# Optimization experiments

Measured on AMD Instinct MI355X. Metric: run time of the kernel, lower is better.

## Reference

```python
import jax, jax.numpy as jnp
from jax import lax
import numpy as np

DN = ('NCHW', 'OIHW', 'NCHW')


def conv3x3(x, w, b):
    y = lax.conv_general_dilated(x, w, (1, 1), ((1, 1), (1, 1)), dimension_numbers=DN)
    return y + b[None, :, None, None]


def box_mean(x, k):
    # Uniform k x k box mean with reflect padding; separable (exactly equal to
    # the dense ones/k^2 conv in the original since the kernel is rank-1).
    pad = k // 2
    C = x.shape[1]
    xp = jnp.pad(x, ((0, 0), (0, 0), (pad, pad), (pad, pad)), mode='reflect')
    kh = jnp.ones((C, 1, k, 1), x.dtype) / k
    kw = jnp.ones((C, 1, 1, k), x.dtype) / k
    y = lax.conv_general_dilated(xp, kh, (1, 1), 'VALID', feature_group_count=C, dimension_numbers=DN)
    y = lax.conv_general_dilated(y, kw, (1, 1), 'VALID', feature_group_count=C, dimension_numbers=DN)
    return y


def std_map_for_window(features, k):
    # features: [N, 8, H, W]
    C = features.shape[1]
    m = box_mean(features, k)
    m2 = box_mean(features * features, k)
    var = jnp.maximum(m2 - m * m, 1e-6)
    w = jax.nn.softmax(jnp.ones((C,), features.dtype))  # uniform (C==8 branch)
    sm = jnp.einsum('nchw,c->nhw', jnp.sqrt(var), w)[:, None]  # [N,1,H,W]
    return jnp.power(sm, 0.8)


def setup_inputs() -> dict:
    key = jax.random.key(0)
    ks = jax.random.split(key, 8)
    B, H, W = 8, 512, 512
    x = jax.random.normal(ks[0], (B, 4, H, W), dtype=jnp.float32)
    s = 0.05
    conv1_w = jax.random.normal(ks[1], (32, 4, 3, 3), jnp.float32) * s
    conv1_b = jnp.zeros((32,), jnp.float32)
    conv2_w = jax.random.normal(ks[2], (16, 32, 3, 3), jnp.float32) * s
    conv2_b = jnp.zeros((16,), jnp.float32)
    conv3_w = jax.random.normal(ks[3], (8, 16, 3, 3), jnp.float32) * s
    conv3_b = jnp.zeros((8,), jnp.float32)
    fusion_w = jnp.full((1, 3, 1, 1), 1.0 / 3.0, jnp.float32)  # init per module
    fusion_b = jnp.zeros((1,), jnp.float32)
    channel_weights = jnp.ones((4,), jnp.float32) / 4.0
    return dict(x=x, conv1_w=conv1_w, conv1_b=conv1_b, conv2_w=conv2_w,
                conv2_b=conv2_b, conv3_w=conv3_w, conv3_b=conv3_b,
                fusion_w=fusion_w, fusion_b=fusion_b,
                channel_weights=channel_weights)


def reference(x, conv1_w, conv1_b, conv2_w, conv2_b, conv3_w, conv3_b,
              fusion_w, fusion_b, channel_weights):
    window_sizes = (11, 25, 49)
    # feature extractor
    f = jax.nn.leaky_relu(conv3x3(x, conv1_w, conv1_b), 0.2)
    f = jax.nn.leaky_relu(conv3x3(f, conv2_w, conv2_b), 0.2)
    f = conv3x3(f, conv3_w, conv3_b)  # [B,8,H,W]
    # multi-scale std maps
    maps = [std_map_for_window(f, k) for k in window_sizes]
    multi = jnp.concatenate(maps, axis=1)  # [B,3,H,W]
    fused = jax.nn.relu(
        lax.conv_general_dilated(multi, fusion_w, (1, 1), 'VALID', dimension_numbers=DN)
        + fusion_b[None, :, None, None])  # [B,1,H,W]
    # adaptive thresholds
    std_flat = fused.ravel()
    q = jnp.quantile(std_flat, jnp.array([0.25, 0.75], fused.dtype))
    q25, q75 = q[0], q[1]
    iqr = q75 - q25
    iqr = jnp.where(iqr < 1e-5, jnp.asarray(0.05, fused.dtype), iqr)
    global_std = jnp.std(x, axis=(2, 3), keepdims=True, ddof=1)  # [B,4,1,1]
    lower = jnp.broadcast_to((q25 - 0.5 * iqr), global_std.shape)
    upper = jnp.broadcast_to((q75 + 0.5 * iqr), global_std.shape)
    gf = jnp.clip(global_std * 5.0, 0.5, 2.0)
    lower = lower * gf
    upper = upper * gf
    cw = jax.nn.softmax(channel_weights).reshape(1, 4, 1, 1)
    channel_std = jnp.std(x * cw, axis=(2, 3), keepdims=True, ddof=1)
    cf = jnp.clip(channel_std * 2.0, 0.8, 1.2)
    lower = lower * cf
    upper = upper * cf
    degenerate = jnp.min(jnp.abs(upper - lower)) < 1e-5
    mean_t = (upper + lower) / 2
    lower = jnp.where(degenerate, mean_t - 0.05, lower)
    upper = jnp.where(degenerate, mean_t + 0.05, upper)
    # texture mask
    diff = jnp.maximum(upper - lower, 1e-5)
    norm = jnp.clip((fused - lower) / diff, 0.0, 1.0)  # [B,4,H,W] via broadcast
    mask = jax.nn.sigmoid(6.0 * norm - 3.0)
    return jnp.mean(mask, axis=1, keepdims=True)  # [B,1,H,W]
```

## Files before the change

### kernel.cpp

```cpp
#include <hip/hip_runtime.h>
#include <hip/hip_bf16.h>
#include <math.h>


template<int CIN, int COUT, int COT, bool LRELU>
__global__ __launch_bounds__(256) void conv3x3_k(
    const float* __restrict__ in,
    const float* __restrict__ wgt,
    const float* __restrict__ bias,
    float* __restrict__ out)
{
    constexpr int TW = 64, TH = 32, CG = COUT / COT, SW = TW + 4;
    __shared__ float sl[(TH + 2) * SW];

    const int tx  = threadIdx.x & 7;
    const int ty  = threadIdx.x >> 3;
    const int x0  = blockIdx.x * TW;
    const int y0  = blockIdx.y * TH;
    const int cog = blockIdx.z % CG;
    const int bb  = blockIdx.z / CG;

    const float* inb = in + (size_t)bb * CIN * 512 * 512;

    float acc[COT][8];
#pragma unroll
    for (int j = 0; j < COT; ++j)
#pragma unroll
        for (int p = 0; p < 8; ++p) acc[j][p] = 0.f;

    for (int ci = 0; ci < CIN; ++ci) {
        __syncthreads();
        const float* ip = inb + (size_t)ci * 512 * 512;
        for (int idx = threadIdx.x; idx < (TH + 2) * (TW + 2); idx += 256) {
            int r  = idx / (TW + 2);
            int cc = idx - r * (TW + 2);
            int yy = y0 - 1 + r, xx = x0 - 1 + cc;
            float v = 0.f;
            if ((unsigned)yy < 512u && (unsigned)xx < 512u) v = ip[yy * 512 + xx];
            sl[r * SW + cc] = v;
        }
        __syncthreads();
        const float* wci = wgt + ((size_t)(cog * COT) * CIN + ci) * 9;
#pragma unroll
        for (int dy = 0; dy < 3; ++dy) {
            const float* rowp = &sl[(ty + dy) * SW + tx * 8];
            float rr[10];
            float4 a0 = *(const float4*)(rowp);
            float4 a1 = *(const float4*)(rowp + 4);
            float2 a2 = *(const float2*)(rowp + 8);
            rr[0]=a0.x; rr[1]=a0.y; rr[2]=a0.z; rr[3]=a0.w;
            rr[4]=a1.x; rr[5]=a1.y; rr[6]=a1.z; rr[7]=a1.w;
            rr[8]=a2.x; rr[9]=a2.y;
#pragma unroll
            for (int j = 0; j < COT; ++j) {
#pragma unroll
                for (int dx = 0; dx < 3; ++dx) {
                    float w = wci[(size_t)j * CIN * 9 + dy * 3 + dx];
#pragma unroll
                    for (int p = 0; p < 8; ++p)
                        acc[j][p] = fmaf(rr[p + dx], w, acc[j][p]);
                }
            }
        }
    }

    const int y = y0 + ty;
#pragma unroll
    for (int j = 0; j < COT; ++j) {
        int co = cog * COT + j;
        float b = bias[co];
        float* op = out + (((size_t)bb * COUT + co) * 512 + y) * 512 + x0 + tx * 8;
        float v[8];
#pragma unroll
        for (int p = 0; p < 8; ++p) {
            float t = acc[j][p] + b;
            if (LRELU) t = t > 0.f ? t : 0.2f * t;
            v[p] = t;
        }
        ((float4*)op)[0] = make_float4(v[0], v[1], v[2], v[3]);
        ((float4*)op)[1] = make_float4(v[4], v[5], v[6], v[7]);
    }
}

__device__ __forceinline__ float2 f2add(float2 a, float2 b) {
    return make_float2(a.x + b.x, a.y + b.y);
}
__device__ __forceinline__ int mir(int v) {
    return v < 0 ? -v : (v > 511 ? 1022 - v : v);
}

#define YB 4

__global__ __launch_bounds__(256) void stdmap_k(
    const float* __restrict__ f,
    const float* __restrict__ fw,
    const float* __restrict__ fbp,
    float* __restrict__ fused,
    int b0)
{
    const int y0   = blockIdx.x * YB;
    const int bb   = blockIdx.y;
    const int t    = threadIdx.x;
    const int lane = t & 63, wid = t >> 6;

    __shared__ float S[3][2][513];
    __shared__ float wtt[4][6];

    const int   RAD[3] = {5, 12, 24};
    const float INV[3] = {1.f/121.f, 1.f/625.f, 1.f/2401.f};

    float smacc[3][YB][2];
#pragma unroll
    for (int sc = 0; sc < 3; ++sc)
#pragma unroll
        for (int yy = 0; yy < YB; ++yy)
            { smacc[sc][yy][0] = 0.f; smacc[sc][yy][1] = 0.f; }

    for (int c = 0; c < 8; ++c) {
        const float* base = f + ((size_t)bb * 8 + c) * 512 * 512;

        float2 wf[3], wq[3];
        {
            float2 sf[3] = {{0.f,0.f},{0.f,0.f},{0.f,0.f}};
            float2 sq[3] = {{0.f,0.f},{0.f,0.f},{0.f,0.f}};
#pragma unroll
            for (int dy = -24; dy <= 24; ++dy) {
                int row = mir(y0 + dy);
                float2 v  = ((const float2*)(base + (size_t)row * 512))[t];
                float2 vq = make_float2(v.x * v.x, v.y * v.y);
                int ad = dy < 0 ? -dy : dy;
                int ring = ad <= 5 ? 0 : (ad <= 12 ? 1 : 2);
                sf[ring] = f2add(sf[ring], v);
                sq[ring] = f2add(sq[ring], vq);
            }
            wf[0] = sf[0];              wq[0] = sq[0];
            wf[1] = f2add(sf[1], wf[0]); wq[1] = f2add(sq[1], wq[0]);
            wf[2] = f2add(sf[2], wf[1]); wq[2] = f2add(sq[2], wq[1]);
        }

        for (int yy = 0; yy < YB; ++yy) {
            const int y = y0 + yy;
            if (yy > 0) {
#pragma unroll
                for (int sc = 0; sc < 3; ++sc) {
                    int ra = mir(y + RAD[sc]);
                    int rs = mir(y - 1 - RAD[sc]);
                    float2 va = ((const float2*)(base + (size_t)ra * 512))[t];
                    float2 vs = ((const float2*)(base + (size_t)rs * 512))[t];
                    wf[sc].x += va.x - vs.x;       wf[sc].y += va.y - vs.y;
                    wq[sc].x += va.x*va.x - vs.x*vs.x;
                    wq[sc].y += va.y*va.y - vs.y*vs.y;
                }
            }

            float pf[3], pq[3], incf[3], incq[3];
#pragma unroll
            for (int sc = 0; sc < 3; ++sc) {
                pf[sc] = wf[sc].x + wf[sc].y;
                pq[sc] = wq[sc].x + wq[sc].y;
                incf[sc] = pf[sc]; incq[sc] = pq[sc];
            }
#pragma unroll
            for (int off = 1; off < 64; off <<= 1) {
#pragma unroll
                for (int sc = 0; sc < 3; ++sc) {
                    float uf = __shfl_up(incf[sc], (unsigned)off, 64);
                    float uq = __shfl_up(incq[sc], (unsigned)off, 64);
                    if (lane >= off) { incf[sc] += uf; incq[sc] += uq; }
                }
            }
            if (lane == 63) {
#pragma unroll
                for (int sc = 0; sc < 3; ++sc) {
                    wtt[wid][sc]     = incf[sc];
                    wtt[wid][3 + sc] = incq[sc];
                }
            }
            __syncthreads();
            float wpf[3] = {0.f,0.f,0.f}, wpq[3] = {0.f,0.f,0.f};
#pragma unroll
            for (int w = 0; w < 4; ++w)
                if (w < wid)
#pragma unroll
                    for (int sc = 0; sc < 3; ++sc) {
                        wpf[sc] += wtt[w][sc];
                        wpq[sc] += wtt[w][3 + sc];
                    }
#pragma unroll
            for (int sc = 0; sc < 3; ++sc) {
                float exf = wpf[sc] + incf[sc] - pf[sc];
                float exq = wpq[sc] + incq[sc] - pq[sc];
                S[sc][0][2*t+1] = exf + wf[sc].x;
                S[sc][0][2*t+2] = exf + pf[sc];
                S[sc][1][2*t+1] = exq + wq[sc].x;
                S[sc][1][2*t+2] = exq + pq[sc];
            }
            if (t == 0)
#pragma unroll
                for (int sc = 0; sc < 3; ++sc)
                    { S[sc][0][0] = 0.f; S[sc][1][0] = 0.f; }
            __syncthreads();

#pragma unroll
            for (int sc = 0; sc < 3; ++sc) {
                const int r = RAD[sc];
                const float* Sf = S[sc][0];
                const float* Sq = S[sc][1];
#pragma unroll
                for (int slot = 0; slot < 2; ++slot) {
                    int xx = 2*t + slot;
                    int lo = xx - r, hi = xx + r;
                    int loc = lo < 0 ? 0 : lo;
                    int hic = hi > 511 ? 511 : hi;
                    float wfv = Sf[hic + 1] - Sf[loc];
                    float wqv = Sq[hic + 1] - Sq[loc];
                    if (lo < 0)   { wfv += Sf[r - xx + 1] - Sf[1];
                                    wqv += Sq[r - xx + 1] - Sq[1]; }
                    if (hi > 511) { wfv += Sf[511] - Sf[1022 - xx - r];
                                    wqv += Sq[511] - Sq[1022 - xx - r]; }
                    float m   = wfv * INV[sc];
                    float m2  = wqv * INV[sc];
                    float var = m2 - m * m;
                    var = var > 1e-6f ? var : 1e-6f;
                    smacc[sc][yy][slot] += sqrtf(var);
                }
            }
            __syncthreads();
        }
    }

    const float w0 = fw[0], w1 = fw[1], w2 = fw[2], b = fbp[0];
#pragma unroll
    for (int yy = 0; yy < YB; ++yy) {
        float o[2];
#pragma unroll
        for (int slot = 0; slot < 2; ++slot) {
            float m0 = powf(smacc[0][yy][slot] * 0.125f, 0.8f);
            float m1 = powf(smacc[1][yy][slot] * 0.125f, 0.8f);
            float m2 = powf(smacc[2][yy][slot] * 0.125f, 0.8f);
            float fv = w0 * m0 + w1 * m1 + w2 * m2 + b;
            o[slot] = fv > 0.f ? fv : 0.f;
        }
        ((float2*)(fused + ((size_t)(b0 + bb) * 512 + y0 + yy) * 512))[t] =
            make_float2(o[0], o[1]);
    }
}

__global__ __launch_bounds__(256) void plane_std_part_k(
    const float* __restrict__ x, double* __restrict__ part)
{
    const int plane = blockIdx.x >> 5;
    const int blk   = blockIdx.x & 31;
    const float* p = x + (size_t)plane * 262144 + (size_t)blk * 8192;
    double s = 0.0, s2 = 0.0;
    for (int i = threadIdx.x; i < 2048; i += 256) {
        float4 v = ((const float4*)p)[i];
        s  += (double)v.x + (double)v.y + (double)v.z + (double)v.w;
        s2 += (double)v.x * v.x + (double)v.y * v.y
            + (double)v.z * v.z + (double)v.w * v.w;
    }
    __shared__ double ls[256], ls2[256];
    ls[threadIdx.x] = s; ls2[threadIdx.x] = s2;
    __syncthreads();
    for (int off = 128; off > 0; off >>= 1) {
        if (threadIdx.x < off) {
            ls[threadIdx.x]  += ls[threadIdx.x + off];
            ls2[threadIdx.x] += ls2[threadIdx.x + off];
        }
        __syncthreads();
    }
    if (threadIdx.x == 0) {
        part[2 * blockIdx.x]     = ls[0];
        part[2 * blockIdx.x + 1] = ls2[0];
    }
}

__global__ void plane_std_fin_k(const double* __restrict__ part,
                                float* __restrict__ stds)
{
    const int plane = threadIdx.x;
    if (plane >= 32) return;
    double s = 0.0, s2 = 0.0;
    for (int b = 0; b < 32; ++b) {
        s  += part[2 * (plane * 32 + b)];
        s2 += part[2 * (plane * 32 + b) + 1];
    }
    const double N = 262144.0;
    double var = (s2 - s * s / N) / (N - 1.0);
    stds[plane] = (float)sqrt(var > 0.0 ? var : 0.0);
}

__global__ __launch_bounds__(256) void hist1_k(
    const float* __restrict__ fused, unsigned* __restrict__ h)
{
    __shared__ unsigned lh[4096];
    for (int i = threadIdx.x; i < 4096; i += 256) lh[i] = 0u;
    __syncthreads();
    const int base = blockIdx.x * 2048;
    for (int i = threadIdx.x; i < 2048; i += 256) {
        unsigned bits = __float_as_uint(fused[base + i]);
        atomicAdd(&lh[bits >> 20], 1u);
    }
    __syncthreads();
    for (int i = threadIdx.x; i < 4096; i += 256) {
        unsigned c = lh[i];
        if (c) atomicAdd(&h[i], c);
    }
}

__global__ __launch_bounds__(256) void select_par_k(
    const unsigned* __restrict__ h, unsigned* __restrict__ pfx,
    unsigned* __restrict__ rem, int level)
{
    const int tt = blockIdx.x;
    const int t = threadIdx.x, lane = t & 63, wid = t >> 6;
    const unsigned targets[4] = {524287u, 524288u, 1572863u, 1572864u};
    const unsigned R = (level == 1) ? targets[tt] : rem[tt];
    const unsigned* hb = (level == 1) ? h : h + tt * 4096;

    unsigned loc[16], lsum = 0;
    const uint4* hv = (const uint4*)(hb + t * 16);
#pragma unroll
    for (int i = 0; i < 4; ++i) {
        uint4 v = hv[i];
        loc[4*i]=v.x; loc[4*i+1]=v.y; loc[4*i+2]=v.z; loc[4*i+3]=v.w;
        lsum += v.x + v.y + v.z + v.w;
    }
    __shared__ unsigned warr[4];
    __shared__ unsigned rbin, rrem;
    unsigned inc = lsum;
#pragma unroll
    for (int off = 1; off < 64; off <<= 1) {
        unsigned up = __shfl_up(inc, (unsigned)off, 64);
        if (lane >= off) inc += up;
    }
    if (lane == 63) warr[wid] = inc;
    __syncthreads();
    unsigned wpre = 0;
#pragma unroll
    for (int w = 0; w < 4; ++w) if (w < wid) wpre += warr[w];
    unsigned ex = wpre + inc - lsum;
    if (R >= ex && R < ex + lsum) {
        unsigned cum = ex;
#pragma unroll
        for (int i = 0; i < 16; ++i) {
            if (cum + loc[i] > R) { rbin = (unsigned)(t * 16 + i); rrem = R - cum; break; }
            cum += loc[i];
        }
    }
    __syncthreads();
    if (t == 0) {
        if (level == 1) { pfx[tt] = rbin << 20; rem[tt] = rrem; }
        else            { pfx[tt] |= rbin << 8; rem[tt] = rrem; }
    }
}

__global__ __launch_bounds__(256) void hist2_k(
    const float* __restrict__ fused, const unsigned* __restrict__ pfx,
    unsigned* __restrict__ h2)
{
    __shared__ unsigned lh[4 * 4096];
    for (int i = threadIdx.x; i < 4 * 4096; i += 256) lh[i] = 0u;
    unsigned p0 = pfx[0] >> 20, p1 = pfx[1] >> 20,
             p2 = pfx[2] >> 20, p3 = pfx[3] >> 20;
    __syncthreads();
    const int base = blockIdx.x * 2048;
    for (int i = threadIdx.x; i < 2048; i += 256) {
        unsigned bits = __float_as_uint(fused[base + i]);
        unsigned top = bits >> 20;
        unsigned mid = (bits >> 8) & 0xFFFu;
        if (top == p0) atomicAdd(&lh[0 * 4096 + mid], 1u);
        if (top == p1) atomicAdd(&lh[1 * 4096 + mid], 1u);
        if (top == p2) atomicAdd(&lh[2 * 4096 + mid], 1u);
        if (top == p3) atomicAdd(&lh[3 * 4096 + mid], 1u);
    }
    __syncthreads();
    for (int i = threadIdx.x; i < 4 * 4096; i += 256) {
        unsigned c = lh[i];
        if (c) atomicAdd(&h2[i], c);
    }
}

__global__ __launch_bounds__(256) void hist3_k(
    const float* __restrict__ fused, const unsigned* __restrict__ pfx,
    unsigned* __restrict__ h3)
{
    __shared__ unsigned lh[4 * 256];
    for (int i = threadIdx.x; i < 4 * 256; i += 256) lh[i] = 0u;
    unsigned p0 = pfx[0] >> 8, p1 = pfx[1] >> 8,
             p2 = pfx[2] >> 8, p3 = pfx[3] >> 8;
    __syncthreads();
    const int base = blockIdx.x * 2048;
    for (int i = threadIdx.x; i < 2048; i += 256) {
        unsigned bits = __float_as_uint(fused[base + i]);
        unsigned top = bits >> 8;
        unsigned low = bits & 0xFFu;
        if (top == p0) atomicAdd(&lh[0 * 256 + low], 1u);
        if (top == p1) atomicAdd(&lh[1 * 256 + low], 1u);
        if (top == p2) atomicAdd(&lh[2 * 256 + low], 1u);
        if (top == p3) atomicAdd(&lh[3 * 256 + low], 1u);
    }
    __syncthreads();
    for (int i = threadIdx.x; i < 4 * 256; i += 256) {
        unsigned c = lh[i];
        if (c) atomicAdd(&h3[i], c);
    }
}

__device__ __forceinline__ float clampf(float v, float lo, float hi) {
    return v < lo ? lo : (v > hi ? hi : v);
}

__global__ __launch_bounds__(256) void finalize_k(
    const unsigned* __restrict__ h3,
    const unsigned* __restrict__ pfx,
    const unsigned* __restrict__ rem,
    const float* __restrict__ stds,
    const float* __restrict__ cw,
    float* __restrict__ lu)
{
    const int tt = threadIdx.x >> 6, lane = threadIdx.x & 63;
    __shared__ float vals[4];

    {
        const unsigned R = rem[tt];
        const unsigned* h = h3 + tt * 256;
        uint4 v = ((const uint4*)h)[lane];
        unsigned loc[4] = {v.x, v.y, v.z, v.w};
        unsigned lsum = v.x + v.y + v.z + v.w;
        unsigned inc = lsum;
#pragma unroll
        for (int off = 1; off < 64; off <<= 1) {
            unsigned up = __shfl_up(inc, (unsigned)off, 64);
            if (lane >= off) inc += up;
        }
        unsigned ex = inc - lsum;
        if (R >= ex && R < ex + lsum) {
            unsigned cum = ex;
#pragma unroll
            for (int i = 0; i < 4; ++i) {
                if (cum + loc[i] > R) {
                    vals[tt] = __uint_as_float(pfx[tt] | (unsigned)(lane * 4 + i));
                    break;
                }
                cum += loc[i];
            }
        }
    }
    __syncthreads();
    if (threadIdx.x != 0) return;

    float q25 = vals[0] + 0.75f * (vals[1] - vals[0]);
    float q75 = vals[2] + 0.25f * (vals[3] - vals[2]);
    float iqr = q75 - q25;
    if (iqr < 1e-5f) iqr = 0.05f;
    float lo0 = q25 - 0.5f * iqr, up0 = q75 + 0.5f * iqr;

    float mx = cw[0];
    for (int c = 1; c < 4; ++c) mx = cw[c] > mx ? cw[c] : mx;
    float e[4], se = 0.f;
    for (int c = 0; c < 4; ++c) { e[c] = expf(cw[c] - mx); se += e[c]; }

    float l[32], u[32], mind = 1e30f;
    for (int p = 0; p < 32; ++p) {
        float sd = stds[p];
        int c = p & 3;
        float gf = clampf(sd * 5.f, 0.5f, 2.f);
        float cf = clampf(sd * (e[c] / se) * 2.f, 0.8f, 1.2f);
        l[p] = lo0 * gf * cf;
        u[p] = up0 * gf * cf;
        float d = fabsf(u[p] - l[p]);
        if (d < mind) mind = d;
    }
    bool deg = mind < 1e-5f;
    for (int p = 0; p < 32; ++p) {
        float L = l[p], U = u[p];
        if (deg) { float m = 0.5f * (L + U); L = m - 0.05f; U = m + 0.05f; }
        lu[p] = L; lu[32 + p] = U;
    }
}

__global__ __launch_bounds__(256) void mask_k(
    const float* __restrict__ fused, const float* __restrict__ lu,
    float* __restrict__ out)
{
    const int b = blockIdx.y;
    const int i = blockIdx.x * 256 + threadIdx.x;
    float fv = fused[(size_t)b * 262144 + i];
    float s = 0.f;
#pragma unroll
    for (int c = 0; c < 4; ++c) {
        float L = lu[b * 4 + c], U = lu[32 + b * 4 + c];
        float d = U - L; d = d > 1e-5f ? d : 1e-5f;
        float n = (fv - L) / d;
        n = n < 0.f ? 0.f : (n > 1.f ? 1.f : n);
        s += 1.f / (1.f + expf(3.f - 6.f * n));
    }
    out[(size_t)b * 262144 + i] = 0.25f * s;
}

extern "C" void kernel_launch(void* const* d_in, const int* in_sizes, int n_in,
                              void* d_out, int out_size, void* d_ws, size_t ws_size,
                              hipStream_t stream)
{
    const float* x   = (const float*)d_in[0];
    const float* c1w = (const float*)d_in[1];
    const float* c1b = (const float*)d_in[2];
    const float* c2w = (const float*)d_in[3];
    const float* c2b = (const float*)d_in[4];
    const float* c3w = (const float*)d_in[5];
    const float* c3b = (const float*)d_in[6];
    const float* fw  = (const float*)d_in[7];
    const float* fb  = (const float*)d_in[8];
    const float* cwt = (const float*)d_in[9];
    float* out = (float*)d_out;
    char* ws = (char*)d_ws;

    const size_t PLANE = 512 * 512;

    float* fused = (float*)ws;
    size_t off = 8 * PLANE * sizeof(float);
    float* stds = (float*)(ws + off); off += 32 * 4;
    float* lu   = (float*)(ws + off); off += 64 * 4;
    off = (off + 255) & ~(size_t)255;
    unsigned* pfx = (unsigned*)(ws + off); off += 16;
    unsigned* rem = (unsigned*)(ws + off); off += 16;
    off = (off + 255) & ~(size_t)255;
    unsigned* h1 = (unsigned*)(ws + off); off += 4096 * 4;
    unsigned* h2 = (unsigned*)(ws + off); off += 4 * 4096 * 4;
    unsigned* h3 = (unsigned*)(ws + off); off += 4 * 256 * 4;
    off = (off + 255) & ~(size_t)255;
    double* part = (double*)(ws + off); off += 1024 * 2 * sizeof(double);
    off = (off + 1023) & ~(size_t)1023;

    const size_t perb = 56 * PLANE * sizeof(float);
    int nb = 8;
    while (nb > 1 && off + (size_t)nb * perb > ws_size) nb >>= 1;
    float* f1  = (float*)(ws + off);
    float* f2  = f1 + (size_t)nb * 32 * PLANE;
    float* fch = f2 + (size_t)nb * 16 * PLANE;

    hipLaunchKernelGGL(plane_std_part_k, dim3(1024), dim3(256), 0, stream, x, part);
    hipLaunchKernelGGL(plane_std_fin_k,  dim3(1),    dim3(64),  0, stream, part, stds);

    for (int b0 = 0; b0 < 8; b0 += nb) {
        const float* xc = x + (size_t)b0 * 4 * PLANE;
        hipLaunchKernelGGL((conv3x3_k<4, 32, 8, true>),   dim3(8, 16, nb * 4),
                           dim3(256), 0, stream, xc, c1w, c1b, f1);
        hipLaunchKernelGGL((conv3x3_k<32, 16, 16, true>), dim3(8, 16, nb),
                           dim3(256), 0, stream, f1, c2w, c2b, f2);
        hipLaunchKernelGGL((conv3x3_k<16, 8, 8, false>),  dim3(8, 16, nb),
                           dim3(256), 0, stream, f2, c3w, c3b, fch);
        hipLaunchKernelGGL(stdmap_k, dim3(512 / YB, nb), dim3(256), 0, stream,
                           fch, fw, fb, fused, b0);
    }

    hipMemsetAsync(h1, 0, (4096 + 4 * 4096 + 4 * 256) * 4, stream);
    hipLaunchKernelGGL(hist1_k,     dim3(1024), dim3(256), 0, stream, fused, h1);
    hipLaunchKernelGGL(select_par_k, dim3(4),   dim3(256), 0, stream, h1, pfx, rem, 1);
    hipLaunchKernelGGL(hist2_k,     dim3(1024), dim3(256), 0, stream, fused, pfx, h2);
    hipLaunchKernelGGL(select_par_k, dim3(4),   dim3(256), 0, stream, h2, pfx, rem, 2);
    hipLaunchKernelGGL(hist3_k,     dim3(1024), dim3(256), 0, stream, fused, pfx, h3);
    hipLaunchKernelGGL(finalize_k,  dim3(1),    dim3(256), 0, stream,
                       h3, pfx, rem, stds, cwt, lu);
    hipLaunchKernelGGL(mask_k, dim3(1024, 8), dim3(256), 0, stream, fused, lu, out);
}
```

Baseline: 1.233 ms.

## Retile conv3x3 to 4 pixels per thread with 4-channel smem batches, remap stdmap blocks

```diff
diff --git a/kernel.cpp b/kernel.cpp
--- a/kernel.cpp
+++ b/kernel.cpp
@@ -4,61 +4,66 @@
 
 
 template<int CIN, int COUT, int COT, bool LRELU>
-__global__ __launch_bounds__(256) void conv3x3_k(
+__global__ __launch_bounds__(256, 4) void conv3x3_k(
     const float* __restrict__ in,
     const float* __restrict__ wgt,
     const float* __restrict__ bias,
     float* __restrict__ out)
 {
-    constexpr int TW = 64, TH = 32, CG = COUT / COT, SW = TW + 4;
-    __shared__ float sl[(TH + 2) * SW];
-
-    const int tx  = threadIdx.x & 7;
-    const int ty  = threadIdx.x >> 3;
+    constexpr int TW = 64, TH = 16, CG = COUT / COT, SW = 68, CB = 4;
+    constexpr int RPC = (TH + 2) * SW;
+    __shared__ float sl[CB * RPC];
+
+    const int tx  = threadIdx.x & 15;
+    const int ty  = threadIdx.x >> 4;
     const int x0  = blockIdx.x * TW;
     const int y0  = blockIdx.y * TH;
     const int cog = blockIdx.z % CG;
     const int bb  = blockIdx.z / CG;
 
-    const float* inb = in + (size_t)bb * CIN * 512 * 512;
-
-    float acc[COT][8];
+    const float* inb = in + (size_t)bb * CIN * 262144;
+
+    float acc[COT][4];
 #pragma unroll
     for (int j = 0; j < COT; ++j)
 #pragma unroll
-        for (int p = 0; p < 8; ++p) acc[j][p] = 0.f;
-
-    for (int ci = 0; ci < CIN; ++ci) {
+        for (int p = 0; p < 4; ++p) acc[j][p] = 0.f;
+
+    for (int cg = 0; cg < CIN / CB; ++cg) {
         __syncthreads();
-        const float* ip = inb + (size_t)ci * 512 * 512;
-        for (int idx = threadIdx.x; idx < (TH + 2) * (TW + 2); idx += 256) {
-            int r  = idx / (TW + 2);
-            int cc = idx - r * (TW + 2);
-            int yy = y0 - 1 + r, xx = x0 - 1 + cc;
-            float v = 0.f;
-            if ((unsigned)yy < 512u && (unsigned)xx < 512u) v = ip[yy * 512 + xx];
-            sl[r * SW + cc] = v;
+        const int ci0 = cg * CB;
+        for (int idx = threadIdx.x; idx < CB * RPC; idx += 256) {
+            int ci  = idx / RPC;
+            int rem = idx - ci * RPC;
+            int r   = rem / SW;
+            int c   = rem - r * SW;
+            if (c < TW + 2) {
+                int yy = y0 - 1 + r, xx = x0 - 1 + c;
+                float v = 0.f;
+                if ((unsigned)yy < 512u && (unsigned)xx < 512u)
+                    v = inb[(size_t)(ci0 + ci) * 262144 + yy * 512 + xx];
+                sl[idx] = v;
+            }
         }
         __syncthreads();
-        const float* wci = wgt + ((size_t)(cog * COT) * CIN + ci) * 9;
-#pragma unroll
-        for (int dy = 0; dy < 3; ++dy) {
-            const float* rowp = &sl[(ty + dy) * SW + tx * 8];
-            float rr[10];
-            float4 a0 = *(const float4*)(rowp);
-            float4 a1 = *(const float4*)(rowp + 4);
-            float2 a2 = *(const float2*)(rowp + 8);
-            rr[0]=a0.x; rr[1]=a0.y; rr[2]=a0.z; rr[3]=a0.w;
-            rr[4]=a1.x; rr[5]=a1.y; rr[6]=a1.z; rr[7]=a1.w;
-            rr[8]=a2.x; rr[9]=a2.y;
-#pragma unroll
-            for (int j = 0; j < COT; ++j) {
-#pragma unroll
-                for (int dx = 0; dx < 3; ++dx) {
-                    float w = wci[(size_t)j * CIN * 9 + dy * 3 + dx];
-#pragma unroll
-                    for (int p = 0; p < 8; ++p)
-                        acc[j][p] = fmaf(rr[p + dx], w, acc[j][p]);
+#pragma unroll
+        for (int ci = 0; ci < CB; ++ci) {
+            const float* wci = wgt + ((size_t)(cog * COT) * CIN + ci0 + ci) * 9;
+#pragma unroll
+            for (int dy = 0; dy < 3; ++dy) {
+                const float* rowp = &sl[ci * RPC + (ty + dy) * SW + tx * 4];
+                float4 a0 = *(const float4*)rowp;
+                float2 a1 = *(const float2*)(rowp + 4);
+                float rr[6] = {a0.x, a0.y, a0.z, a0.w, a1.x, a1.y};
+#pragma unroll
+                for (int j = 0; j < COT; ++j) {
+#pragma unroll
+                    for (int dx = 0; dx < 3; ++dx) {
+                        float w = wci[(size_t)j * CIN * 9 + dy * 3 + dx];
+#pragma unroll
+                        for (int p = 0; p < 4; ++p)
+                            acc[j][p] = fmaf(rr[p + dx], w, acc[j][p]);
+                    }
                 }
             }
         }
@@ -69,16 +74,15 @@
     for (int j = 0; j < COT; ++j) {
         int co = cog * COT + j;
         float b = bias[co];
-        float* op = out + (((size_t)bb * COUT + co) * 512 + y) * 512 + x0 + tx * 8;
-        float v[8];
-#pragma unroll
-        for (int p = 0; p < 8; ++p) {
+        float* op = out + (((size_t)bb * COUT + co) * 512 + y) * 512 + x0 + tx * 4;
+        float v[4];
+#pragma unroll
+        for (int p = 0; p < 4; ++p) {
             float t = acc[j][p] + b;
             if (LRELU) t = t > 0.f ? t : 0.2f * t;
             v[p] = t;
         }
         ((float4*)op)[0] = make_float4(v[0], v[1], v[2], v[3]);
-        ((float4*)op)[1] = make_float4(v[4], v[5], v[6], v[7]);
     }
 }
 
@@ -98,8 +102,11 @@
     float* __restrict__ fused,
     int b0)
 {
-    const int y0   = blockIdx.x * YB;
-    const int bb   = blockIdx.y;
+    const int total = gridDim.x * gridDim.y;
+    const int lin   = blockIdx.y * gridDim.x + blockIdx.x;
+    const int task  = (lin & 7) * (total >> 3) + (lin >> 3);
+    const int bb    = task >> 7;
+    const int y0    = (task & 127) * YB;
     const int t    = threadIdx.x;
     const int lane = t & 63, wid = t >> 6;
 
@@ -545,11 +552,11 @@
 
     for (int b0 = 0; b0 < 8; b0 += nb) {
         const float* xc = x + (size_t)b0 * 4 * PLANE;
-        hipLaunchKernelGGL((conv3x3_k<4, 32, 8, true>),   dim3(8, 16, nb * 4),
+        hipLaunchKernelGGL((conv3x3_k<4, 32, 16, true>),  dim3(8, 32, nb * 2),
                            dim3(256), 0, stream, xc, c1w, c1b, f1);
-        hipLaunchKernelGGL((conv3x3_k<32, 16, 16, true>), dim3(8, 16, nb),
+        hipLaunchKernelGGL((conv3x3_k<32, 16, 16, true>), dim3(8, 32, nb),
                            dim3(256), 0, stream, f1, c2w, c2b, f2);
-        hipLaunchKernelGGL((conv3x3_k<16, 8, 8, false>),  dim3(8, 16, nb),
+        hipLaunchKernelGGL((conv3x3_k<16, 8, 8, false>),  dim3(8, 32, nb),
                            dim3(256), 0, stream, f2, c3w, c3b, fch);
         hipLaunchKernelGGL(stdmap_k, dim3(512 / YB, nb), dim3(256), 0, stream,
                            fch, fw, fb, fused, b0);
```

Measured after the change: 1.327 ms. 1.08x slower.

## Fuse conv1 into conv2 via shared-memory recompute and swizzle stdmap block order

Applied to the files above, without the earlier changes.

```diff
diff --git a/kernel.cpp b/kernel.cpp
--- a/kernel.cpp
+++ b/kernel.cpp
@@ -3,34 +3,159 @@
 #include <math.h>
 
 
-template<int CIN, int COUT, int COT, bool LRELU>
-__global__ __launch_bounds__(256) void conv3x3_k(
+__global__ __launch_bounds__(256, 2) void conv12_k(
+    const float* __restrict__ x,
+    const float* __restrict__ w1,
+    const float* __restrict__ b1,
+    const float* __restrict__ w2,
+    const float* __restrict__ b2,
+    float* __restrict__ f2)
+{
+    __shared__ float xs[4 * 36 * 68];
+    __shared__ float f1s[4 * 34 * 68];
+
+    const int t  = threadIdx.x;
+    const int tx = t & 7;
+    const int ty = t >> 3;
+    const int x0 = blockIdx.x * 64;
+    const int y0 = blockIdx.y * 32;
+    const int bb = blockIdx.z;
+    const float* xb = x + (size_t)bb * 4 * 262144;
+
+    for (int i = t; i < 9792; i += 256) {
+        int ci  = i / 2448;
+        int rem = i - ci * 2448;
+        int r   = rem / 68;
+        int c   = rem - r * 68;
+        int Y = y0 - 2 + r, X = x0 - 2 + c;
+        float v = 0.f;
+        if ((unsigned)Y < 512u && (unsigned)X < 512u)
+            v = xb[ci * 262144 + Y * 512 + X];
+        xs[i] = v;
+    }
+
+    float acc[16][8];
+#pragma unroll
+    for (int j = 0; j < 16; ++j)
+#pragma unroll
+        for (int p = 0; p < 8; ++p) acc[j][p] = 0.f;
+
+    for (int g = 0; g < 8; ++g) {
+        __syncthreads();
+
+#pragma unroll
+        for (int fc = 0; fc < 4; ++fc) {
+            const int foc = g * 4 + fc;
+            float wv[36];
+#pragma unroll
+            for (int k = 0; k < 36; ++k) wv[k] = w1[foc * 36 + k];
+            const float bias = b1[foc];
+            for (int it = t; it < 578; it += 256) {
+                int r  = it / 17;
+                int q  = it - r * 17;
+                int c0 = q * 4;
+                int Y1 = y0 - 1 + r;
+                float v[4] = {bias, bias, bias, bias};
+#pragma unroll
+                for (int ci = 0; ci < 4; ++ci) {
+#pragma unroll
+                    for (int ky = 0; ky < 3; ++ky) {
+                        const float* xr = &xs[ci * 2448 + (r + ky) * 68 + c0];
+                        float4 a  = *(const float4*)xr;
+                        float2 bl = *(const float2*)(xr + 4);
+                        float rr[6] = {a.x, a.y, a.z, a.w, bl.x, bl.y};
+#pragma unroll
+                        for (int kx = 0; kx < 3; ++kx) {
+                            float w = wv[ci * 9 + ky * 3 + kx];
+#pragma unroll
+                            for (int p = 0; p < 4; ++p)
+                                v[p] = fmaf(rr[p + kx], w, v[p]);
+                        }
+                    }
+                }
+                float st[4];
+                bool rowok = ((unsigned)Y1 < 512u);
+#pragma unroll
+                for (int p = 0; p < 4; ++p) {
+                    int X1 = x0 - 1 + c0 + p;
+                    bool ok = rowok && ((unsigned)X1 < 512u) && (c0 + p <= 65);
+                    float tv = v[p];
+                    tv = tv > 0.f ? tv : 0.2f * tv;
+                    st[p] = ok ? tv : 0.f;
+                }
+                *(float4*)&f1s[fc * 2312 + r * 68 + c0] =
+                    make_float4(st[0], st[1], st[2], st[3]);
+            }
+        }
+        __syncthreads();
+
+#pragma unroll
+        for (int fc = 0; fc < 4; ++fc) {
+            const int ci = g * 4 + fc;
+#pragma unroll
+            for (int dy = 0; dy < 3; ++dy) {
+                const float* rowp = &f1s[fc * 2312 + (ty + dy) * 68 + tx * 8];
+                float4 a0 = *(const float4*)(rowp);
+                float4 a1 = *(const float4*)(rowp + 4);
+                float2 a2 = *(const float2*)(rowp + 8);
+                float rr[10] = {a0.x, a0.y, a0.z, a0.w,
+                                a1.x, a1.y, a1.z, a1.w, a2.x, a2.y};
+#pragma unroll
+                for (int j = 0; j < 16; ++j) {
+#pragma unroll
+                    for (int dx = 0; dx < 3; ++dx) {
+                        float w = w2[(j * 32 + ci) * 9 + dy * 3 + dx];
+#pragma unroll
+                        for (int p = 0; p < 8; ++p)
+                            acc[j][p] = fmaf(rr[p + dx], w, acc[j][p]);
+                    }
+                }
+            }
+        }
+    }
+
+    const int y = y0 + ty;
+#pragma unroll
+    for (int j = 0; j < 16; ++j) {
+        float b = b2[j];
+        float* op = f2 + (((size_t)bb * 16 + j) * 512 + y) * 512 + x0 + tx * 8;
+        float v[8];
+#pragma unroll
+        for (int p = 0; p < 8; ++p) {
+            float tv = acc[j][p] + b;
+            v[p] = tv > 0.f ? tv : 0.2f * tv;
+        }
+        ((float4*)op)[0] = make_float4(v[0], v[1], v[2], v[3]);
+        ((float4*)op)[1] = make_float4(v[4], v[5], v[6], v[7]);
+    }
+}
+
+__global__ __launch_bounds__(256) void conv3_k(
     const float* __restrict__ in,
     const float* __restrict__ wgt,
     const float* __restrict__ bias,
     float* __restrict__ out)
 {
-    constexpr int TW = 64, TH = 32, CG = COUT / COT, SW = TW + 4;
+    constexpr int TW = 64, TH = 32, SW = TW + 4;
     __shared__ float sl[(TH + 2) * SW];
 
-    const int tx  = threadIdx.x & 7;
-    const int ty  = threadIdx.x >> 3;
-    const int x0  = blockIdx.x * TW;
-    const int y0  = blockIdx.y * TH;
-    const int cog = blockIdx.z % CG;
-    const int bb  = blockIdx.z / CG;
-
-    const float* inb = in + (size_t)bb * CIN * 512 * 512;
-
-    float acc[COT][8];
-#pragma unroll
-    for (int j = 0; j < COT; ++j)
+    const int tx = threadIdx.x & 7;
+    const int ty = threadIdx.x >> 3;
+    const int x0 = blockIdx.x * TW;
+    const int y0 = blockIdx.y * TH;
+    const int bb = blockIdx.z;
+
+    const float* inb = in + (size_t)bb * 16 * 262144;
+
+    float acc[8][8];
+#pragma unroll
+    for (int j = 0; j < 8; ++j)
 #pragma unroll
         for (int p = 0; p < 8; ++p) acc[j][p] = 0.f;
 
-    for (int ci = 0; ci < CIN; ++ci) {
+    for (int ci = 0; ci < 16; ++ci) {
         __syncthreads();
-        const float* ip = inb + (size_t)ci * 512 * 512;
+        const float* ip = inb + (size_t)ci * 262144;
         for (int idx = threadIdx.x; idx < (TH + 2) * (TW + 2); idx += 256) {
             int r  = idx / (TW + 2);
             int cc = idx - r * (TW + 2);
@@ -40,22 +165,20 @@
             sl[r * SW + cc] = v;
         }
         __syncthreads();
-        const float* wci = wgt + ((size_t)(cog * COT) * CIN + ci) * 9;
+        const float* wci = wgt + (size_t)ci * 9;
 #pragma unroll
         for (int dy = 0; dy < 3; ++dy) {
             const float* rowp = &sl[(ty + dy) * SW + tx * 8];
-            float rr[10];
             float4 a0 = *(const float4*)(rowp);
             float4 a1 = *(const float4*)(rowp + 4);
             float2 a2 = *(const float2*)(rowp + 8);
-            rr[0]=a0.x; rr[1]=a0.y; rr[2]=a0.z; rr[3]=a0.w;
-            rr[4]=a1.x; rr[5]=a1.y; rr[6]=a1.z; rr[7]=a1.w;
-            rr[8]=a2.x; rr[9]=a2.y;
-#pragma unroll
-            for (int j = 0; j < COT; ++j) {
+            float rr[10] = {a0.x, a0.y, a0.z, a0.w,
+                            a1.x, a1.y, a1.z, a1.w, a2.x, a2.y};
+#pragma unroll
+            for (int j = 0; j < 8; ++j) {
 #pragma unroll
                 for (int dx = 0; dx < 3; ++dx) {
-                    float w = wci[(size_t)j * CIN * 9 + dy * 3 + dx];
+                    float w = wci[(size_t)j * 16 * 9 + dy * 3 + dx];
 #pragma unroll
                     for (int p = 0; p < 8; ++p)
                         acc[j][p] = fmaf(rr[p + dx], w, acc[j][p]);
@@ -66,17 +189,12 @@
 
     const int y = y0 + ty;
 #pragma unroll
-    for (int j = 0; j < COT; ++j) {
-        int co = cog * COT + j;
-        float b = bias[co];
-        float* op = out + (((size_t)bb * COUT + co) * 512 + y) * 512 + x0 + tx * 8;
+    for (int j = 0; j < 8; ++j) {
+        float b = bias[j];
+        float* op = out + (((size_t)bb * 8 + j) * 512 + y) * 512 + x0 + tx * 8;
         float v[8];
 #pragma unroll
-        for (int p = 0; p < 8; ++p) {
-            float t = acc[j][p] + b;
-            if (LRELU) t = t > 0.f ? t : 0.2f * t;
-            v[p] = t;
-        }
+        for (int p = 0; p < 8; ++p) v[p] = acc[j][p] + b;
         ((float4*)op)[0] = make_float4(v[0], v[1], v[2], v[3]);
         ((float4*)op)[1] = make_float4(v[4], v[5], v[6], v[7]);
     }
@@ -98,8 +216,11 @@
     float* __restrict__ fused,
     int b0)
 {
-    const int y0   = blockIdx.x * YB;
-    const int bb   = blockIdx.y;
+    const int total = gridDim.x * gridDim.y;
+    const int lin   = blockIdx.y * gridDim.x + blockIdx.x;
+    const int task  = (lin & 7) * (total >> 3) + (lin >> 3);
+    const int bb    = task >> 7;
+    const int y0    = (task & 127) * YB;
     const int t    = threadIdx.x;
     const int lane = t & 63, wid = t >> 6;
 
@@ -133,7 +254,7 @@
                 sf[ring] = f2add(sf[ring], v);
                 sq[ring] = f2add(sq[ring], vq);
             }
-            wf[0] = sf[0];              wq[0] = sq[0];
+            wf[0] = sf[0];               wq[0] = sq[0];
             wf[1] = f2add(sf[1], wf[0]); wq[1] = f2add(sq[1], wq[0]);
             wf[2] = f2add(sf[2], wf[1]); wq[2] = f2add(sq[2], wq[1]);
         }
@@ -533,11 +654,10 @@
     double* part = (double*)(ws + off); off += 1024 * 2 * sizeof(double);
     off = (off + 1023) & ~(size_t)1023;
 
-    const size_t perb = 56 * PLANE * sizeof(float);
+    const size_t perb = 24 * PLANE * sizeof(float);
     int nb = 8;
     while (nb > 1 && off + (size_t)nb * perb > ws_size) nb >>= 1;
-    float* f1  = (float*)(ws + off);
-    float* f2  = f1 + (size_t)nb * 32 * PLANE;
+    float* f2  = (float*)(ws + off);
     float* fch = f2 + (size_t)nb * 16 * PLANE;
 
     hipLaunchKernelGGL(plane_std_part_k, dim3(1024), dim3(256), 0, stream, x, part);
@@ -545,12 +665,10 @@
 
     for (int b0 = 0; b0 < 8; b0 += nb) {
         const float* xc = x + (size_t)b0 * 4 * PLANE;
-        hipLaunchKernelGGL((conv3x3_k<4, 32, 8, true>),   dim3(8, 16, nb * 4),
-                           dim3(256), 0, stream, xc, c1w, c1b, f1);
-        hipLaunchKernelGGL((conv3x3_k<32, 16, 16, true>), dim3(8, 16, nb),
-                           dim3(256), 0, stream, f1, c2w, c2b, f2);
-        hipLaunchKernelGGL((conv3x3_k<16, 8, 8, false>),  dim3(8, 16, nb),
-                           dim3(256), 0, stream, f2, c3w, c3b, fch);
+        hipLaunchKernelGGL(conv12_k, dim3(8, 16, nb), dim3(256), 0, stream,
+                           xc, c1w, c1b, c2w, c2b, f2);
+        hipLaunchKernelGGL(conv3_k,  dim3(8, 16, nb), dim3(256), 0, stream,
+                           f2, c3w, c3b, fch);
         hipLaunchKernelGGL(stdmap_k, dim3(512 / YB, nb), dim3(256), 0, stream,
                            fch, fw, fb, fused, b0);
     }
```

Result: faster. 1.114 ms (-9.6%).
